# Kernel tuning notes

Measured on AMD Instinct MI355X. Metric: run time of the kernel, lower is better.

Reference implementation:

```python
import jax, jax.numpy as jnp
import numpy as np

N, C, H, W = 32, 512, 64, 64
R = 16
CB = C // R  # bottleneck channels = 32
EPS = 1e-5


def setup_inputs() -> dict:
    key = jax.random.key(0)
    ks = jax.random.split(key, 5)
    return {
        "x": jax.random.normal(ks[0], (N, C, H, W), dtype=jnp.float32),
        "wk_w": jax.random.normal(ks[1], (C,), dtype=jnp.float32) * (1.0 / np.sqrt(C)),
        "wk_b": jax.random.normal(ks[2], (1,), dtype=jnp.float32) * 0.01,
        "wv1_w": jax.random.normal(ks[3], (CB, C), dtype=jnp.float32) * (1.0 / np.sqrt(C)),
        "ln_g": jnp.ones((CB,), dtype=jnp.float32),
        "ln_b": jnp.zeros((CB,), dtype=jnp.float32),
        "wv2_w": jax.random.normal(ks[4], (C, CB), dtype=jnp.float32) * (1.0 / np.sqrt(CB)),
    }


def reference(x, wk_w, wk_b, wv1_w, ln_g, ln_b, wv2_w):
    # x: (n, c, h, w)
    # attention logits via 1x1 conv (c -> 1): (n, h, w)
    logits = jnp.einsum("nchw,c->nhw", x, wk_w) + wk_b[0]
    # Faithful to original: F.softmax(dim=2) on (n,1,h,w) -> softmax over H only
    attn = jax.nn.softmax(logits, axis=1)  # (n, h, w)
    # context pooling: (n, c, hw) @ (n, hw, 1) -> (n, c)
    ctx = jnp.einsum("nchw,nhw->nc", x, attn)
    # bottleneck: conv1x1 (c -> c/r), LayerNorm over channel, ReLU, conv1x1 (c/r -> c)
    v = ctx @ wv1_w.T  # (n, c/r)
    mu = jnp.mean(v, axis=-1, keepdims=True)
    var = jnp.mean((v - mu) ** 2, axis=-1, keepdims=True)
    v = (v - mu) * jax.lax.rsqrt(var + EPS) * ln_g + ln_b
    v = jax.nn.relu(v)
    out = v @ wv2_w.T  # (n, c)
    return out[:, :, None, None] + x
```

## Files before the change

### kernel.cpp

```cpp
#include <hip/hip_runtime.h>

#define N 32
#define C 512
#define H 64
#define W 64
#define HW 4096
#define CB 32
#define NCHUNK 8
#define CCHUNK 64
#define EPS 1e-5f

typedef float fvec4 __attribute__((ext_vector_type(4)));

__global__ __launch_bounds__(256) void k1_logits_partial(
    const float* __restrict__ x, const float* __restrict__ wk_w,
    float* __restrict__ partial)
{
    const int tid   = threadIdx.x;
    const int hw4   = blockIdx.x * 256 + tid;
    const int chunk = blockIdx.y;
    const int n     = blockIdx.z;
    const int c0    = chunk * CCHUNK;
    const float4* xb = (const float4*)(x + ((size_t)n * C + c0) * HW);
    float4 acc = make_float4(0.f, 0.f, 0.f, 0.f);
    #pragma unroll 8
    for (int c = 0; c < CCHUNK; ++c) {
        const float wv = wk_w[c0 + c];
        const float4 xv = xb[(size_t)c * (HW / 4) + hw4];
        acc.x += xv.x * wv; acc.y += xv.y * wv;
        acc.z += xv.z * wv; acc.w += xv.w * wv;
    }
    float4* pb = (float4*)(partial + (size_t)(n * NCHUNK + chunk) * HW);
    pb[hw4] = acc;
}

__global__ __launch_bounds__(256) void k2_softmax(
    const float* __restrict__ partial, const float* __restrict__ wk_b,
    float* __restrict__ attn)
{
    const int tid  = threadIdx.x;
    const int lane = tid & 63;
    const int wid  = blockIdx.x * 4 + (tid >> 6);
    const int n = wid >> 6;
    const int w = wid & 63;
    float l = wk_b[0];
    #pragma unroll
    for (int ch = 0; ch < NCHUNK; ++ch)
        l += partial[(size_t)(n * NCHUNK + ch) * HW + lane * W + w];
    float m = l;
    #pragma unroll
    for (int o = 32; o > 0; o >>= 1) m = fmaxf(m, __shfl_xor(m, o));
    const float e = __expf(l - m);
    float s = e;
    #pragma unroll
    for (int o = 32; o > 0; o >>= 1) s += __shfl_xor(s, o);
    attn[(size_t)n * HW + lane * W + w] = e / s;
}

__global__ __launch_bounds__(256) void k3_ctx(
    const float* __restrict__ x, const float* __restrict__ attn,
    float* __restrict__ ctx)
{
    const int tid  = threadIdx.x;
    const int lane = tid & 63;
    const int g    = blockIdx.x * 4 + (tid >> 6);
    const int n    = g >> 7;
    const int c0   = (g & 127) * 4;
    const float4* ar = (const float4*)(attn + (size_t)n * HW);
    const float4* xr = (const float4*)(x + ((size_t)n * C + c0) * HW);
    float a0 = 0.f, a1 = 0.f, a2 = 0.f, a3 = 0.f;
    #pragma unroll
    for (int i = 0; i < 16; ++i) {
        const int idx = i * 64 + lane;
        const float4 av = ar[idx];
        const float4 x0 = xr[idx];
        const float4 x1 = xr[1024 + idx];
        const float4 x2 = xr[2048 + idx];
        const float4 x3 = xr[3072 + idx];
        a0 += x0.x * av.x + x0.y * av.y + x0.z * av.z + x0.w * av.w;
        a1 += x1.x * av.x + x1.y * av.y + x1.z * av.z + x1.w * av.w;
        a2 += x2.x * av.x + x2.y * av.y + x2.z * av.z + x2.w * av.w;
        a3 += x3.x * av.x + x3.y * av.y + x3.z * av.z + x3.w * av.w;
    }
    #pragma unroll
    for (int o = 32; o > 0; o >>= 1) {
        a0 += __shfl_xor(a0, o);
        a1 += __shfl_xor(a1, o);
        a2 += __shfl_xor(a2, o);
        a3 += __shfl_xor(a3, o);
    }
    if (lane == 0) {
        *(float4*)(ctx + (size_t)n * C + c0) = make_float4(a0, a1, a2, a3);
    }
}

__global__ __launch_bounds__(256) void k4_bottleneck(
    const float* __restrict__ ctx, const float* __restrict__ wv1_w,
    const float* __restrict__ ln_g, const float* __restrict__ ln_b,
    const float* __restrict__ wv2_w, float* __restrict__ out_vec)
{
    __shared__ float ctx_s[C];
    __shared__ float v_s[CB];
    const int tid = threadIdx.x;
    const int n   = blockIdx.x;
    ctx_s[tid]       = ctx[n * C + tid];
    ctx_s[tid + 256] = ctx[n * C + tid + 256];
    __syncthreads();
    {
        const int b = tid >> 3, sub = tid & 7;
        const float* wr = wv1_w + b * C;
        float s = 0.f;
        #pragma unroll 8
        for (int j = sub; j < C; j += 8) s += wr[j] * ctx_s[j];
        #pragma unroll
        for (int o = 4; o > 0; o >>= 1) s += __shfl_down(s, o, 8);
        if (sub == 0) v_s[b] = s;
    }
    __syncthreads();
    if (tid < CB) {
        const float val = v_s[tid];
        float sm = val, sq = val * val;
        #pragma unroll
        for (int o = 16; o > 0; o >>= 1) {
            sm += __shfl_xor(sm, o, 32);
            sq += __shfl_xor(sq, o, 32);
        }
        const float mu  = sm / CB;
        const float var = sq / CB - mu * mu;
        const float vh  = (val - mu) * rsqrtf(var + EPS) * ln_g[tid] + ln_b[tid];
        v_s[tid] = fmaxf(vh, 0.f);
    }
    __syncthreads();
    for (int c = tid; c < C; c += 256) {
        const float* w2 = wv2_w + c * CB;
        float a = 0.f;
        #pragma unroll
        for (int b = 0; b < CB; ++b) a += v_s[b] * w2[b];
        out_vec[n * C + c] = a;
    }
}

__global__ __launch_bounds__(256) void k5_add(
    const float* __restrict__ x, const float* __restrict__ out_vec,
    float* __restrict__ out)
{
    const int tid = threadIdx.x;
    const int nc  = blockIdx.x;
    const fvec4* xp = (const fvec4*)x + (size_t)nc * (HW / 4);
    fvec4*       op = (fvec4*)out     + (size_t)nc * (HW / 4);
    const float a = out_vec[nc];
    #pragma unroll
    for (int i = 0; i < 4; ++i) {
        const int idx = i * 256 + tid;
        fvec4 v = __builtin_nontemporal_load(xp + idx);
        v += a;
        __builtin_nontemporal_store(v, op + idx);
    }
}

extern "C" void kernel_launch(void* const* d_in, const int* in_sizes, int n_in,
                              void* d_out, int out_size, void* d_ws, size_t ws_size,
                              hipStream_t stream) {
    const float* x     = (const float*)d_in[0];
    const float* wk_w  = (const float*)d_in[1];
    const float* wk_b  = (const float*)d_in[2];
    const float* wv1_w = (const float*)d_in[3];
    const float* ln_g  = (const float*)d_in[4];
    const float* ln_b  = (const float*)d_in[5];
    const float* wv2_w = (const float*)d_in[6];
    float* out = (float*)d_out;

    float* ws      = (float*)d_ws;
    float* partial = ws;
    float* attn    = partial + (size_t)N * NCHUNK * HW;
    float* ctx     = attn + (size_t)N * HW;
    float* ovec    = ctx + (size_t)N * C;

    k1_logits_partial<<<dim3(4, NCHUNK, 32), 256, 0, stream>>>(x, wk_w, partial);
    k2_softmax<<<512, 256, 0, stream>>>(partial, wk_b, attn);
    k3_ctx<<<1024, 256, 0, stream>>>(x, attn, ctx);
    k4_bottleneck<<<32, 256, 0, stream>>>(ctx, wv1_w, ln_g, ln_b, wv2_w, ovec);
    k5_add<<<16384, 256, 0, stream>>>(x, ovec, out);
}
```

Measured before the change: 543.1 us.

## Retile logits and context kernels into 16-channel chunks over full spatial plane

The logits kernel now has each block cover 16 channels across the whole 4096-element plane, with four float4 accumulators per thread. This raises the partial-sum count to 32 chunks per sample. The context kernel uses the same tiling: each thread keeps its attention values in registers and reuses them across 16 channels, then reduces per channel with wave shuffles and shared memory. The aim is fewer redundant attention loads and more independent loads in flight per thread. The cost is that the softmax kernel now reads four times as much partial data, and the launch grids change shape.

```diff
diff --git a/kernel.cpp b/kernel.cpp
--- a/kernel.cpp
+++ b/kernel.cpp
@@ -6,32 +6,37 @@
 #define W 64
 #define HW 4096
 #define CB 32
-#define NCHUNK 8
-#define CCHUNK 64
+#define CCH 16
+#define NCHUNK 32
 #define EPS 1e-5f
 
 typedef float fvec4 __attribute__((ext_vector_type(4)));
 
-__global__ __launch_bounds__(256) void k1_logits_partial(
+__global__ __launch_bounds__(256) void k1_logits(
     const float* __restrict__ x, const float* __restrict__ wk_w,
     float* __restrict__ partial)
 {
     const int tid   = threadIdx.x;
-    const int hw4   = blockIdx.x * 256 + tid;
-    const int chunk = blockIdx.y;
-    const int n     = blockIdx.z;
-    const int c0    = chunk * CCHUNK;
+    const int chunk = blockIdx.x;
+    const int n     = blockIdx.y;
+    const int c0    = chunk * CCH;
     const float4* xb = (const float4*)(x + ((size_t)n * C + c0) * HW);
-    float4 acc = make_float4(0.f, 0.f, 0.f, 0.f);
-    #pragma unroll 8
-    for (int c = 0; c < CCHUNK; ++c) {
+    float4 acc[4];
+    #pragma unroll
+    for (int i = 0; i < 4; ++i) acc[i] = make_float4(0.f, 0.f, 0.f, 0.f);
+    #pragma unroll 4
+    for (int c = 0; c < CCH; ++c) {
         const float wv = wk_w[c0 + c];
-        const float4 xv = xb[(size_t)c * (HW / 4) + hw4];
-        acc.x += xv.x * wv; acc.y += xv.y * wv;
-        acc.z += xv.z * wv; acc.w += xv.w * wv;
+        #pragma unroll
+        for (int i = 0; i < 4; ++i) {
+            const float4 xv = xb[c * 1024 + i * 256 + tid];
+            acc[i].x += xv.x * wv; acc[i].y += xv.y * wv;
+            acc[i].z += xv.z * wv; acc[i].w += xv.w * wv;
+        }
     }
-    float4* pb = (float4*)(partial + (size_t)(n * NCHUNK + chunk) * HW);
-    pb[hw4] = acc;
+    float4* pb = (float4*)(partial + ((size_t)n * NCHUNK + chunk) * HW);
+    #pragma unroll
+    for (int i = 0; i < 4; ++i) pb[i * 256 + tid] = acc[i];
 }
 
 __global__ __launch_bounds__(256) void k2_softmax(
@@ -46,7 +51,7 @@
     float l = wk_b[0];
     #pragma unroll
     for (int ch = 0; ch < NCHUNK; ++ch)
-        l += partial[(size_t)(n * NCHUNK + ch) * HW + lane * W + w];
+        l += partial[((size_t)n * NCHUNK + ch) * HW + lane * W + w];
     float m = l;
     #pragma unroll
     for (int o = 32; o > 0; o >>= 1) m = fmaxf(m, __shfl_xor(m, o));
@@ -61,36 +66,42 @@
     const float* __restrict__ x, const float* __restrict__ attn,
     float* __restrict__ ctx)
 {
-    const int tid  = threadIdx.x;
-    const int lane = tid & 63;
-    const int g    = blockIdx.x * 4 + (tid >> 6);
-    const int n    = g >> 7;
-    const int c0   = (g & 127) * 4;
+    const int tid   = threadIdx.x;
+    const int chunk = blockIdx.x;
+    const int n     = blockIdx.y;
+    const int c0    = chunk * CCH;
     const float4* ar = (const float4*)(attn + (size_t)n * HW);
-    const float4* xr = (const float4*)(x + ((size_t)n * C + c0) * HW);
-    float a0 = 0.f, a1 = 0.f, a2 = 0.f, a3 = 0.f;
+    const float4* xb = (const float4*)(x + ((size_t)n * C + c0) * HW);
+    float4 av[4];
     #pragma unroll
-    for (int i = 0; i < 16; ++i) {
-        const int idx = i * 64 + lane;
-        const float4 av = ar[idx];
-        const float4 x0 = xr[idx];
-        const float4 x1 = xr[1024 + idx];
-        const float4 x2 = xr[2048 + idx];
-        const float4 x3 = xr[3072 + idx];
-        a0 += x0.x * av.x + x0.y * av.y + x0.z * av.z + x0.w * av.w;
-        a1 += x1.x * av.x + x1.y * av.y + x1.z * av.z + x1.w * av.w;
-        a2 += x2.x * av.x + x2.y * av.y + x2.z * av.z + x2.w * av.w;
-        a3 += x3.x * av.x + x3.y * av.y + x3.z * av.z + x3.w * av.w;
+    for (int i = 0; i < 4; ++i) av[i] = ar[i * 256 + tid];
+    float s[CCH];
+    #pragma unroll
+    for (int c = 0; c < CCH; ++c) s[c] = 0.f;
+    #pragma unroll 4
+    for (int c = 0; c < CCH; ++c) {
+        float t = 0.f;
+        #pragma unroll
+        for (int i = 0; i < 4; ++i) {
+            const float4 xv = xb[c * 1024 + i * 256 + tid];
+            t += xv.x * av[i].x + xv.y * av[i].y
+               + xv.z * av[i].z + xv.w * av[i].w;
+        }
+        s[c] = t;
     }
+    __shared__ float red[CCH][4];
+    const int lane = tid & 63, wv = tid >> 6;
     #pragma unroll
-    for (int o = 32; o > 0; o >>= 1) {
-        a0 += __shfl_xor(a0, o);
-        a1 += __shfl_xor(a1, o);
-        a2 += __shfl_xor(a2, o);
-        a3 += __shfl_xor(a3, o);
+    for (int c = 0; c < CCH; ++c) {
+        float t = s[c];
+        #pragma unroll
+        for (int o = 32; o > 0; o >>= 1) t += __shfl_xor(t, o);
+        if (lane == 0) red[c][wv] = t;
     }
-    if (lane == 0) {
-        *(float4*)(ctx + (size_t)n * C + c0) = make_float4(a0, a1, a2, a3);
+    __syncthreads();
+    if (tid < CCH) {
+        ctx[(size_t)n * C + c0 + tid] =
+            red[tid][0] + red[tid][1] + red[tid][2] + red[tid][3];
     }
 }
 
@@ -176,9 +187,9 @@
     float* ctx     = attn + (size_t)N * HW;
     float* ovec    = ctx + (size_t)N * C;
 
-    k1_logits_partial<<<dim3(4, NCHUNK, 32), 256, 0, stream>>>(x, wk_w, partial);
+    k1_logits<<<dim3(NCHUNK, N), 256, 0, stream>>>(x, wk_w, partial);
     k2_softmax<<<512, 256, 0, stream>>>(partial, wk_b, attn);
-    k3_ctx<<<1024, 256, 0, stream>>>(x, attn, ctx);
+    k3_ctx<<<dim3(NCHUNK, N), 256, 0, stream>>>(x, attn, ctx);
     k4_bottleneck<<<32, 256, 0, stream>>>(ctx, wv1_w, ln_g, ln_b, wv2_w, ovec);
     k5_add<<<16384, 256, 0, stream>>>(x, ovec, out);
 }
```

Measured after the change: 576.0 us. +6.1%, slower.
